# Performance work log

Measured on AMD Instinct MI355X. Metric: run time of the kernel, lower is better.

## Reference

```python
import jax, jax.numpy as jnp
import numpy as np

B, N, C, H = 2, 65536, 96, 3   # 256x256 grid, Swin-T stage-1 dims
R, S = 256, 256                # 256 Voronoi regions of 256 points each


def _block_labels():
    # 16x16 grid of 16x16 blocks over the 256x256 image -> labels 1..256
    r = jnp.arange(256) // 16
    lbl = (r[:, None] * 16 + r[None, :] + 1).astype(jnp.int32)  # [256,256]
    return jnp.broadcast_to(lbl[None], (B, 256, 256))


def setup_inputs() -> dict:
    key = jax.random.key(0)
    ks = jax.random.split(key, 6)
    return {
        "xq": jax.random.normal(ks[0], (B, N, C), jnp.float32),
        "xk": jax.random.normal(ks[1], (B, N, C), jnp.float32),
        "xv": jax.random.normal(ks[2], (B, N, C), jnp.float32),
        "Wq": jax.random.normal(ks[3], (C, C), jnp.float32) * 0.02,
        "bq": jnp.zeros((C,), jnp.float32),
        "Wp": jax.random.normal(ks[4], (C, C), jnp.float32) * 0.02,
        "bp": jnp.zeros((C,), jnp.float32),
        "Voronoi": _block_labels(),
    }


def _attn(xq, xk, xv, Wq, bq, Wp, bp, V):
    hd = C // H
    scale = hd ** -0.5
    # NOTE: source applies self.q to q, k AND v (repo bug) -> shared Wq/bq
    def qkv(x):
        return (x @ Wq + bq).reshape(B, N, H, hd).transpose(0, 2, 1, 3)  # [B,H,N,hd]
    q = qkv(xq) * scale
    k = qkv(xk)
    v = qkv(xv)
    Vf = V.reshape(B, N)

    def per_batch(qb, kb, vb, vor):  # qb: [H,N,hd]
        perm = jnp.argsort(vor)           # group points by region id (stable)
        idx = perm.reshape(R, S)          # uniform region sizes by construction
        qg = qb[:, idx, :]                # [H,R,S,hd]
        kg = kb[:, idx, :]
        vg = vb[:, idx, :]
        attn = jax.nn.softmax(jnp.einsum('hrsd,hrtd->hrst', qg, kg), axis=-1)
        og = jnp.einsum('hrst,hrtd->hrsd', attn, vg).reshape(H, N, hd)
        # scatter back to original token order
        return jnp.zeros_like(qb).at[:, perm, :].set(og)

    x = jax.vmap(per_batch)(q, k, v, Vf)          # [B,H,N,hd]
    x = x.transpose(0, 2, 1, 3).reshape(B, N, C)
    return x @ Wp + bp


def reference(xq, xk, xv, Wq, bq, Wp, bp, Voronoi):
    return _attn(xq, xk, xv, Wq, bq, Wp, bp, Voronoi)
```

## Files before the change

### kernel.cpp

```cpp
#include <hip/hip_runtime.h>
#include <hip/hip_bf16.h>
#include <hip/hip_fp16.h>

#define Bn 2
#define Nn 65536
#define Cn 96
#define Hn 3
#define HD 32

typedef _Float16 half8  __attribute__((ext_vector_type(8)));
typedef _Float16 half4v __attribute__((ext_vector_type(4)));
typedef float    float4v __attribute__((ext_vector_type(4)));

#define MFMA16(a, b, c) __builtin_amdgcn_mfma_f32_16x16x32_f16((a), (b), (c), 0, 0, 0)

__device__ __forceinline__ int member_n(int g, int t) {
    return ((g >> 4) << 12) | ((t >> 4) << 8) | ((g & 15) << 4) | (t & 15);
}

__global__ __launch_bounds__(256) void prep_kernel(const float* __restrict__ Wq,
                                                   const float* __restrict__ Wp,
                                                   _Float16* __restrict__ WqT,
                                                   _Float16* __restrict__ WpT) {
    int i = blockIdx.x * 256 + threadIdx.x;
    if (i < 9216) {
        int n = i / 96, k = i % 96;
        WqT[i] = (_Float16)Wq[k * 96 + n];
    } else {
        int o = i - 9216;
        int n = o / 96, k = o % 96;
        WpT[o] = (_Float16)Wp[k * 96 + n];
    }
}

__global__ __launch_bounds__(256, 2) void fused_kernel(
    const float* __restrict__ xq, const float* __restrict__ xk,
    const float* __restrict__ xv, const _Float16* __restrict__ WqT,
    const _Float16* __restrict__ WpT, const float* __restrict__ bq,
    const float* __restrict__ bp, float* __restrict__ out) {
    __shared__ __align__(16) _Float16 Klds[256 * 40];
    __shared__ __align__(16) _Float16 Vlds[32 * 264];
    __shared__ __align__(16) _Float16 Wscr[4 * 64 * 40];

    const int g = blockIdx.x, b = blockIdx.y;
    const int tid = threadIdx.x;
    const int w = tid >> 6, lane = tid & 63;
    const int q_ = lane >> 4, c16 = lane & 15;
    _Float16* sw = Wscr + w * (64 * 40);
    float* swf = (float*)sw;

    const int tbase = w * 64;
    const float SCALE = 0.17677669529663687f;

    float4v oacc[4][6];
    const float4v z = {0.f, 0.f, 0.f, 0.f};
#pragma unroll
    for (int mt = 0; mt < 4; ++mt)
#pragma unroll
        for (int nt = 0; nt < 6; ++nt) oacc[mt][nt] = z;

    for (int h = 0; h < 3; ++h) {
        if (h) __syncthreads();
        half8 bfq[2][3];
#pragma unroll
        for (int nt2 = 0; nt2 < 2; ++nt2)
#pragma unroll
            for (int kt = 0; kt < 3; ++kt)
                bfq[nt2][kt] = *(const half8*)(WqT + ((2 * h + nt2) * 16 + c16) * 96 + kt * 32 + q_ * 8);
        const float bqv0 = bq[h * 32 + c16];
        const float bqv1 = bq[h * 32 + 16 + c16];

#pragma unroll
        for (int src = 0; src < 2; ++src) {
            const float* X = src ? xv : xk;
            half8 af[4][3];
#pragma unroll
            for (int mt = 0; mt < 4; ++mt) {
                const float* xr = X + ((size_t)b * Nn + member_n(g, tbase + mt * 16 + c16)) * Cn;
#pragma unroll
                for (int kt = 0; kt < 3; ++kt) {
                    const float4v f0 = *(const float4v*)(xr + kt * 32 + q_ * 8);
                    const float4v f1 = *(const float4v*)(xr + kt * 32 + q_ * 8 + 4);
                    half8 a;
                    a[0] = (_Float16)f0[0]; a[1] = (_Float16)f0[1];
                    a[2] = (_Float16)f0[2]; a[3] = (_Float16)f0[3];
                    a[4] = (_Float16)f1[0]; a[5] = (_Float16)f1[1];
                    a[6] = (_Float16)f1[2]; a[7] = (_Float16)f1[3];
                    af[mt][kt] = a;
                }
            }
#pragma unroll
            for (int nt2 = 0; nt2 < 2; ++nt2) {
                const int d = nt2 * 16 + c16;
                const float bias = nt2 ? bqv1 : bqv0;
#pragma unroll
                for (int mt = 0; mt < 4; ++mt) {
                    float4v acc = z;
#pragma unroll
                    for (int kt = 0; kt < 3; ++kt) acc = MFMA16(af[mt][kt], bfq[nt2][kt], acc);
                    const int t0 = tbase + mt * 16 + 4 * q_;
                    if (src == 0) {
#pragma unroll
                        for (int r = 0; r < 4; ++r)
                            Klds[(t0 + r) * 40 + d] = (_Float16)(acc[r] + bias);
                    } else {
                        half4v pk;
#pragma unroll
                        for (int r = 0; r < 4; ++r) pk[r] = (_Float16)(acc[r] + bias);
                        *(half4v*)(Vlds + d * 264 + t0) = pk;
                    }
                }
            }
        }
        __syncthreads();

        {
            half8 af[4][3];
#pragma unroll
            for (int mt = 0; mt < 4; ++mt) {
                const float* xr = xq + ((size_t)b * Nn + member_n(g, tbase + mt * 16 + c16)) * Cn;
#pragma unroll
                for (int kt = 0; kt < 3; ++kt) {
                    const float4v f0 = *(const float4v*)(xr + kt * 32 + q_ * 8);
                    const float4v f1 = *(const float4v*)(xr + kt * 32 + q_ * 8 + 4);
                    half8 a;
                    a[0] = (_Float16)f0[0]; a[1] = (_Float16)f0[1];
                    a[2] = (_Float16)f0[2]; a[3] = (_Float16)f0[3];
                    a[4] = (_Float16)f1[0]; a[5] = (_Float16)f1[1];
                    a[6] = (_Float16)f1[2]; a[7] = (_Float16)f1[3];
                    af[mt][kt] = a;
                }
            }
#pragma unroll
            for (int nt2 = 0; nt2 < 2; ++nt2) {
                const float bias = nt2 ? bqv1 : bqv0;
#pragma unroll
                for (int mt = 0; mt < 4; ++mt) {
                    float4v acc = z;
#pragma unroll
                    for (int kt = 0; kt < 3; ++kt) acc = MFMA16(af[mt][kt], bfq[nt2][kt], acc);
#pragma unroll
                    for (int r = 0; r < 4; ++r)
                        sw[(mt * 16 + 4 * q_ + r) * 40 + nt2 * 16 + c16] =
                            (_Float16)((acc[r] + bias) * SCALE);
                }
            }
        }
        half8 qfrag[4];
#pragma unroll
        for (int mt = 0; mt < 4; ++mt)
            qfrag[mt] = *(const half8*)(sw + (mt * 16 + c16) * 40 + q_ * 8);

        float4v o[4][2];
        float lsum[4][4];
#pragma unroll
        for (int mt = 0; mt < 4; ++mt) {
            o[mt][0] = z; o[mt][1] = z;
#pragma unroll
            for (int r = 0; r < 4; ++r) lsum[mt][r] = 0.f;
        }
        for (int jc = 0; jc < 8; ++jc) {
            const half8 kf0 = *(const half8*)(Klds + (jc * 32 + c16) * 40 + q_ * 8);
            const half8 kf1 = *(const half8*)(Klds + (jc * 32 + 16 + c16) * 40 + q_ * 8);
#pragma unroll
            for (int mt = 0; mt < 4; ++mt) {
#pragma unroll
                for (int jt2 = 0; jt2 < 2; ++jt2) {
                    float4v sv = MFMA16(qfrag[mt], jt2 ? kf1 : kf0, z);
#pragma unroll
                    for (int r = 0; r < 4; ++r) {
                        float p = __expf(sv[r]);
                        lsum[mt][r] += p;
                        sw[(mt * 16 + 4 * q_ + r) * 40 + jt2 * 16 + c16] = (_Float16)p;
                    }
                }
            }
            const half8 vf0 = *(const half8*)(Vlds + c16 * 264 + jc * 32 + q_ * 8);
            const half8 vf1 = *(const half8*)(Vlds + (16 + c16) * 264 + jc * 32 + q_ * 8);
#pragma unroll
            for (int mt = 0; mt < 4; ++mt) {
                const half8 pf = *(const half8*)(sw + (mt * 16 + c16) * 40 + q_ * 8);
                o[mt][0] = MFMA16(pf, vf0, o[mt][0]);
                o[mt][1] = MFMA16(pf, vf1, o[mt][1]);
            }
        }
#pragma unroll
        for (int mt = 0; mt < 4; ++mt)
#pragma unroll
            for (int r = 0; r < 4; ++r) {
                float s = lsum[mt][r];
                s += __shfl_xor(s, 1);  s += __shfl_xor(s, 2);
                s += __shfl_xor(s, 4);  s += __shfl_xor(s, 8);
                lsum[mt][r] = 1.0f / s;
            }

#pragma unroll
        for (int mt = 0; mt < 4; ++mt)
#pragma unroll
            for (int nt2 = 0; nt2 < 2; ++nt2)
#pragma unroll
                for (int r = 0; r < 4; ++r)
                    sw[(mt * 16 + 4 * q_ + r) * 40 + nt2 * 16 + c16] =
                        (_Float16)(o[mt][nt2][r] * lsum[mt][r]);
        half8 afx[4];
#pragma unroll
        for (int mt = 0; mt < 4; ++mt)
            afx[mt] = *(const half8*)(sw + (mt * 16 + c16) * 40 + q_ * 8);
#pragma unroll
        for (int nt = 0; nt < 6; ++nt) {
            const half8 wpb = *(const half8*)(WpT + (nt * 16 + c16) * 96 + h * 32 + q_ * 8);
#pragma unroll
            for (int mt = 0; mt < 4; ++mt)
                oacc[mt][nt] = MFMA16(afx[mt], wpb, oacc[mt][nt]);
        }
    }

    float bpv[6];
#pragma unroll
    for (int nt = 0; nt < 6; ++nt) bpv[nt] = bp[nt * 16 + c16];
#pragma unroll
    for (int mt = 0; mt < 4; ++mt) {
        const int n0 = member_n(g, tbase + mt * 16);
        float* orow = out + ((size_t)b * Nn + n0) * Cn;
#pragma unroll
        for (int p = 0; p < 2; ++p) {
#pragma unroll
            for (int ntl = 0; ntl < 3; ++ntl) {
                const int nt = 3 * p + ntl;
#pragma unroll
                for (int r = 0; r < 4; ++r)
                    swf[(4 * q_ + r) * 52 + ntl * 16 + c16] = oacc[mt][nt][r] + bpv[nt];
            }
            __builtin_amdgcn_s_waitcnt(0);
#pragma unroll
            for (int i = 0; i < 3; ++i) {
                const int f = i * 256 + lane * 4;
                const int t = f / 48, c = f % 48;
                const float4v v = *(const float4v*)(swf + t * 52 + c);
                *(float4v*)(orow + t * 96 + p * 48 + c) = v;
            }
        }
    }
}

extern "C" void kernel_launch(void* const* d_in, const int* in_sizes, int n_in,
                              void* d_out, int out_size, void* d_ws, size_t ws_size,
                              hipStream_t stream) {
    (void)in_sizes; (void)n_in; (void)out_size; (void)ws_size;
    const float* xq = (const float*)d_in[0];
    const float* xk = (const float*)d_in[1];
    const float* xv = (const float*)d_in[2];
    const float* Wq = (const float*)d_in[3];
    const float* bq = (const float*)d_in[4];
    const float* Wp = (const float*)d_in[5];
    const float* bp = (const float*)d_in[6];

    char* ws = (char*)d_ws;
    _Float16* WqT = (_Float16*)(ws + 0);
    _Float16* WpT = (_Float16*)(ws + 20480);

    prep_kernel<<<72, 256, 0, stream>>>(Wq, Wp, WqT, WpT);
    fused_kernel<<<dim3(256, Bn), 256, 0, stream>>>(xq, xk, xv, WqT, WpT, bq, bp,
                                                    (float*)d_out);
}
```

Before: 258.8 us.

## Split region work over 8 waves with double-buffered P scratch and direct stores

The fused kernel now runs each 256-point region with 512 threads (8 waves of 32 rows each) instead of 4 waves of 64 rows. This halves per-wave register arrays and raises the wave count per region, aiming to hide latency better. The per-wave probability scratch is double-buffered across key chunks, and the LDS-staged coalesced output store is replaced by direct per-lane strided global stores. The direct stores are less coalesced and may cost store bandwidth, and the higher launch-bounds occupancy request tightens the register budget.

```diff
diff --git a/kernel.cpp b/kernel.cpp
--- a/kernel.cpp
+++ b/kernel.cpp
@@ -33,29 +33,28 @@
     }
 }
 
-__global__ __launch_bounds__(256, 2) void fused_kernel(
+__global__ __launch_bounds__(512, 4) void fused_kernel(
     const float* __restrict__ xq, const float* __restrict__ xk,
     const float* __restrict__ xv, const _Float16* __restrict__ WqT,
     const _Float16* __restrict__ WpT, const float* __restrict__ bq,
     const float* __restrict__ bp, float* __restrict__ out) {
     __shared__ __align__(16) _Float16 Klds[256 * 40];
     __shared__ __align__(16) _Float16 Vlds[32 * 264];
-    __shared__ __align__(16) _Float16 Wscr[4 * 64 * 40];
+    __shared__ __align__(16) _Float16 Wscr[8 * 2 * 32 * 40];
 
     const int g = blockIdx.x, b = blockIdx.y;
     const int tid = threadIdx.x;
     const int w = tid >> 6, lane = tid & 63;
     const int q_ = lane >> 4, c16 = lane & 15;
-    _Float16* sw = Wscr + w * (64 * 40);
-    float* swf = (float*)sw;
-
-    const int tbase = w * 64;
+    _Float16* sw0 = Wscr + w * 2560;
+
+    const int tbase = w * 32;
     const float SCALE = 0.17677669529663687f;
 
-    float4v oacc[4][6];
+    float4v oacc[2][6];
     const float4v z = {0.f, 0.f, 0.f, 0.f};
 #pragma unroll
-    for (int mt = 0; mt < 4; ++mt)
+    for (int mt = 0; mt < 2; ++mt)
 #pragma unroll
         for (int nt = 0; nt < 6; ++nt) oacc[mt][nt] = z;
 
@@ -73,9 +72,9 @@
 #pragma unroll
         for (int src = 0; src < 2; ++src) {
             const float* X = src ? xv : xk;
-            half8 af[4][3];
-#pragma unroll
-            for (int mt = 0; mt < 4; ++mt) {
+            half8 af[2][3];
+#pragma unroll
+            for (int mt = 0; mt < 2; ++mt) {
                 const float* xr = X + ((size_t)b * Nn + member_n(g, tbase + mt * 16 + c16)) * Cn;
 #pragma unroll
                 for (int kt = 0; kt < 3; ++kt) {
@@ -94,7 +93,7 @@
                 const int d = nt2 * 16 + c16;
                 const float bias = nt2 ? bqv1 : bqv0;
 #pragma unroll
-                for (int mt = 0; mt < 4; ++mt) {
+                for (int mt = 0; mt < 2; ++mt) {
                     float4v acc = z;
 #pragma unroll
                     for (int kt = 0; kt < 3; ++kt) acc = MFMA16(af[mt][kt], bfq[nt2][kt], acc);
@@ -115,9 +114,9 @@
         __syncthreads();
 
         {
-            half8 af[4][3];
-#pragma unroll
-            for (int mt = 0; mt < 4; ++mt) {
+            half8 af[2][3];
+#pragma unroll
+            for (int mt = 0; mt < 2; ++mt) {
                 const float* xr = xq + ((size_t)b * Nn + member_n(g, tbase + mt * 16 + c16)) * Cn;
 #pragma unroll
                 for (int kt = 0; kt < 3; ++kt) {
@@ -135,35 +134,36 @@
             for (int nt2 = 0; nt2 < 2; ++nt2) {
                 const float bias = nt2 ? bqv1 : bqv0;
 #pragma unroll
-                for (int mt = 0; mt < 4; ++mt) {
+                for (int mt = 0; mt < 2; ++mt) {
                     float4v acc = z;
 #pragma unroll
                     for (int kt = 0; kt < 3; ++kt) acc = MFMA16(af[mt][kt], bfq[nt2][kt], acc);
 #pragma unroll
                     for (int r = 0; r < 4; ++r)
-                        sw[(mt * 16 + 4 * q_ + r) * 40 + nt2 * 16 + c16] =
+                        sw0[(mt * 16 + 4 * q_ + r) * 40 + nt2 * 16 + c16] =
                             (_Float16)((acc[r] + bias) * SCALE);
                 }
             }
         }
-        half8 qfrag[4];
-#pragma unroll
-        for (int mt = 0; mt < 4; ++mt)
-            qfrag[mt] = *(const half8*)(sw + (mt * 16 + c16) * 40 + q_ * 8);
-
-        float4v o[4][2];
-        float lsum[4][4];
-#pragma unroll
-        for (int mt = 0; mt < 4; ++mt) {
+        half8 qfrag[2];
+#pragma unroll
+        for (int mt = 0; mt < 2; ++mt)
+            qfrag[mt] = *(const half8*)(sw0 + (mt * 16 + c16) * 40 + q_ * 8);
+
+        float4v o[2][2];
+        float lsum[2][4];
+#pragma unroll
+        for (int mt = 0; mt < 2; ++mt) {
             o[mt][0] = z; o[mt][1] = z;
 #pragma unroll
             for (int r = 0; r < 4; ++r) lsum[mt][r] = 0.f;
         }
         for (int jc = 0; jc < 8; ++jc) {
+            _Float16* sp = sw0 + (jc & 1) * 1280;
             const half8 kf0 = *(const half8*)(Klds + (jc * 32 + c16) * 40 + q_ * 8);
             const half8 kf1 = *(const half8*)(Klds + (jc * 32 + 16 + c16) * 40 + q_ * 8);
 #pragma unroll
-            for (int mt = 0; mt < 4; ++mt) {
+            for (int mt = 0; mt < 2; ++mt) {
 #pragma unroll
                 for (int jt2 = 0; jt2 < 2; ++jt2) {
                     float4v sv = MFMA16(qfrag[mt], jt2 ? kf1 : kf0, z);
@@ -171,21 +171,21 @@
                     for (int r = 0; r < 4; ++r) {
                         float p = __expf(sv[r]);
                         lsum[mt][r] += p;
-                        sw[(mt * 16 + 4 * q_ + r) * 40 + jt2 * 16 + c16] = (_Float16)p;
+                        sp[(mt * 16 + 4 * q_ + r) * 40 + jt2 * 16 + c16] = (_Float16)p;
                     }
                 }
             }
             const half8 vf0 = *(const half8*)(Vlds + c16 * 264 + jc * 32 + q_ * 8);
             const half8 vf1 = *(const half8*)(Vlds + (16 + c16) * 264 + jc * 32 + q_ * 8);
 #pragma unroll
-            for (int mt = 0; mt < 4; ++mt) {
-                const half8 pf = *(const half8*)(sw + (mt * 16 + c16) * 40 + q_ * 8);
+            for (int mt = 0; mt < 2; ++mt) {
+                const half8 pf = *(const half8*)(sp + (mt * 16 + c16) * 40 + q_ * 8);
                 o[mt][0] = MFMA16(pf, vf0, o[mt][0]);
                 o[mt][1] = MFMA16(pf, vf1, o[mt][1]);
             }
         }
 #pragma unroll
-        for (int mt = 0; mt < 4; ++mt)
+        for (int mt = 0; mt < 2; ++mt)
 #pragma unroll
             for (int r = 0; r < 4; ++r) {
                 float s = lsum[mt][r];
@@ -195,22 +195,22 @@
             }
 
 #pragma unroll
-        for (int mt = 0; mt < 4; ++mt)
+        for (int mt = 0; mt < 2; ++mt)
 #pragma unroll
             for (int nt2 = 0; nt2 < 2; ++nt2)
 #pragma unroll
                 for (int r = 0; r < 4; ++r)
-                    sw[(mt * 16 + 4 * q_ + r) * 40 + nt2 * 16 + c16] =
+                    sw0[(mt * 16 + 4 * q_ + r) * 40 + nt2 * 16 + c16] =
                         (_Float16)(o[mt][nt2][r] * lsum[mt][r]);
-        half8 afx[4];
-#pragma unroll
-        for (int mt = 0; mt < 4; ++mt)
-            afx[mt] = *(const half8*)(sw + (mt * 16 + c16) * 40 + q_ * 8);
+        half8 afx[2];
+#pragma unroll
+        for (int mt = 0; mt < 2; ++mt)
+            afx[mt] = *(const half8*)(sw0 + (mt * 16 + c16) * 40 + q_ * 8);
 #pragma unroll
         for (int nt = 0; nt < 6; ++nt) {
             const half8 wpb = *(const half8*)(WpT + (nt * 16 + c16) * 96 + h * 32 + q_ * 8);
 #pragma unroll
-            for (int mt = 0; mt < 4; ++mt)
+            for (int mt = 0; mt < 2; ++mt)
                 oacc[mt][nt] = MFMA16(afx[mt], wpb, oacc[mt][nt]);
         }
     }
@@ -219,27 +219,14 @@
 #pragma unroll
     for (int nt = 0; nt < 6; ++nt) bpv[nt] = bp[nt * 16 + c16];
 #pragma unroll
-    for (int mt = 0; mt < 4; ++mt) {
+    for (int mt = 0; mt < 2; ++mt) {
         const int n0 = member_n(g, tbase + mt * 16);
         float* orow = out + ((size_t)b * Nn + n0) * Cn;
 #pragma unroll
-        for (int p = 0; p < 2; ++p) {
-#pragma unroll
-            for (int ntl = 0; ntl < 3; ++ntl) {
-                const int nt = 3 * p + ntl;
-#pragma unroll
-                for (int r = 0; r < 4; ++r)
-                    swf[(4 * q_ + r) * 52 + ntl * 16 + c16] = oacc[mt][nt][r] + bpv[nt];
-            }
-            __builtin_amdgcn_s_waitcnt(0);
-#pragma unroll
-            for (int i = 0; i < 3; ++i) {
-                const int f = i * 256 + lane * 4;
-                const int t = f / 48, c = f % 48;
-                const float4v v = *(const float4v*)(swf + t * 52 + c);
-                *(float4v*)(orow + t * 96 + p * 48 + c) = v;
-            }
-        }
+        for (int nt = 0; nt < 6; ++nt)
+#pragma unroll
+            for (int r = 0; r < 4; ++r)
+                orow[(4 * q_ + r) * Cn + nt * 16 + c16] = oacc[mt][nt][r] + bpv[nt];
     }
 }
 
@@ -260,6 +247,6 @@
     _Float16* WpT = (_Float16*)(ws + 20480);
 
     prep_kernel<<<72, 256, 0, stream>>>(Wq, Wp, WqT, WpT);
-    fused_kernel<<<dim3(256, Bn), 256, 0, stream>>>(xq, xk, xv, WqT, WpT, bq, bp,
+    fused_kernel<<<dim3(256, Bn), 512, 0, stream>>>(xq, xk, xv, WqT, WpT, bq, bp,
                                                     (float*)d_out);
 }
```

Result: no change. 262.1 us (+1.3%).
